# Kernel optimization log

Measured on AMD Instinct MI355X. Metric: run time of the kernel, lower is better.

## Reference

```python
import jax, jax.numpy as jnp
import numpy as np

H = 16          # num_attention_heads
HD = 64         # attention_head_size
ALPHA = 1.5
BANDWIDTH = 1.0
A_EXP = 0.5     # sinkhorn-like exponent 'a'
DIST_SCALE = float(HD)  # alpha < 2 => scale by head_size
EPS = 1e-12     # F.normalize eps


def setup_inputs() -> dict:
    key = jax.random.key(0)
    ks = jax.random.split(key, 5)
    B, L, D = 2, 1024, 1024
    w_scale = 0.02  # keep distances in a non-degenerate range for the power-law kernel
    x = jax.random.normal(ks[0], (B, L, D), dtype=jnp.float32)
    WQ = jax.random.normal(ks[1], (D, D), dtype=jnp.float32) * w_scale
    WK = jax.random.normal(ks[2], (D, D), dtype=jnp.float32) * w_scale
    WV = jax.random.normal(ks[3], (D, D), dtype=jnp.float32) * w_scale
    WO = jax.random.normal(ks[4], (D, D), dtype=jnp.float32) * w_scale
    z = jnp.zeros((D,), dtype=jnp.float32)
    return {"x": x, "WQ": WQ, "bQ": z, "WK": WK, "bK": z,
            "WV": WV, "bV": z, "WO": WO, "bO": z}


def _heads(t, B, L):
    # [B, L, H*HD] -> [B, H, L, HD]
    return t.reshape(B, L, H, HD).transpose(0, 2, 1, 3)


def reference(x, WQ, bQ, WK, bK, WV, bV, WO, bO):
    B, L, D = x.shape
    q = _heads(x @ WQ + bQ, B, L)   # [B,H,L,HD]
    k = _heads(x @ WK + bK, B, L)
    v = _heads(x @ WV + bV, B, L)

    # torch.cdist(q, k, p=2): pairwise euclidean distance [B,H,L,L]
    q2 = jnp.sum(q * q, axis=-1)                      # [B,H,L]
    k2 = jnp.sum(k * k, axis=-1)                      # [B,H,L]
    qk = jnp.einsum('bhid,bhjd->bhij', q, k)          # [B,H,L,L]
    d2 = q2[..., :, None] + k2[..., None, :] - 2.0 * qk
    g_dist = jnp.sqrt(jnp.maximum(d2, EPS)) / DIST_SCALE

    # alpha < 2: power-law kernel (1 + g/sqrt(bw))^(-(d_intrinsic + alpha))
    attn_score = (1.0 + g_dist / np.sqrt(BANDWIDTH)) ** (-(HD + ALPHA))

    # a > 0: Sinkhorn-style row/col renormalization
    N_R = jnp.sum(attn_score, axis=-1)                # [B,H,L] row sums
    N_C = jnp.sum(attn_score, axis=-2)                # [B,H,L] col sums
    K_tilde = (N_R ** (-A_EXP))[..., :, None] * attn_score * (N_C ** (-A_EXP))[..., None, :]

    # F.normalize(p=1, dim=3); entries are positive so |.| sum == sum
    attention_probs = K_tilde / jnp.maximum(jnp.sum(K_tilde, axis=-1, keepdims=True), EPS)

    out = jnp.einsum('bhij,bhjd->bhid', attention_probs, v)   # [B,H,L,HD]
    out = out.transpose(0, 2, 1, 3).reshape(B, L, H * HD)
    return out @ WO + bO
```

## Files before the change

### kernel.cpp

```cpp
#include <hip/hip_runtime.h>
#include <math.h>


typedef __attribute__((ext_vector_type(8))) short short8;
typedef __attribute__((ext_vector_type(4))) float f32x4;

__device__ inline unsigned short f2bf(float f) {
  unsigned int u = __float_as_uint(f);
  unsigned int r = (u + 0x7FFFu + ((u >> 16) & 1u)) >> 16;
  return (unsigned short)r;
}
__device__ inline float bf2f(unsigned short s) {
  return __uint_as_float(((unsigned int)s) << 16);
}
__device__ inline float score_fn(float dot, float sq) {
  float d2 = fmaxf(fmaf(-2.f, dot, sq), 1e-12f);
  float sd = __builtin_amdgcn_sqrtf(d2);
  float lg = __builtin_amdgcn_logf(fmaf(sd, 0.015625f, 1.0f));
  return __builtin_amdgcn_exp2f(-65.5f * lg);
}
__device__ inline unsigned int cvtpk(float lo, float hi) {
  unsigned int r;
  asm("v_cvt_pk_bf16_f32 %0, %1, %2" : "=v"(r) : "v"(lo), "v"(hi));
  return r;
}
#define GLD16(lptr, gptr)                                                      \
  __builtin_amdgcn_global_load_lds(                                            \
      (const __attribute__((address_space(1))) void*)(gptr),                   \
      (__attribute__((address_space(3))) void*)(lptr), 16, 0, 0)

__global__ __launch_bounds__(256) void cvt_f32_bf16(const float* __restrict__ in,
                                                    unsigned short* __restrict__ out) {
  int i = blockIdx.x * 256 + threadIdx.x;
  float4 v = ((const float4*)in)[i];
  out[4 * i + 0] = f2bf(v.x);
  out[4 * i + 1] = f2bf(v.y);
  out[4 * i + 2] = f2bf(v.z);
  out[4 * i + 3] = f2bf(v.w);
}

__global__ __launch_bounds__(256) void wtrans4(const float* __restrict__ W0,
                                               const float* __restrict__ W1,
                                               const float* __restrict__ W2,
                                               const float* __restrict__ W3,
                                               unsigned short* __restrict__ T0,
                                               unsigned short* __restrict__ T1,
                                               unsigned short* __restrict__ T2,
                                               unsigned short* __restrict__ T3) {
  int z = blockIdx.z;
  const float* W = z == 0 ? W0 : z == 1 ? W1 : z == 2 ? W2 : W3;
  unsigned short* WT = z == 0 ? T0 : z == 1 ? T1 : z == 2 ? T2 : T3;
  __shared__ float T[32][33];
  int k0 = blockIdx.x * 32, n0 = blockIdx.y * 32;
  int c = threadIdx.x & 31, r8 = threadIdx.x >> 5;
#pragma unroll
  for (int it = 0; it < 4; ++it) {
    int rr = r8 + it * 8;
    T[rr][c] = W[(size_t)(k0 + rr) * 1024 + n0 + c];
  }
  __syncthreads();
#pragma unroll
  for (int it = 0; it < 4; ++it) {
    int rr = r8 + it * 8;
    WT[(size_t)(n0 + rr) * 1024 + k0 + c] = f2bf(T[c][rr]);
  }
}

__global__ __launch_bounds__(512, 2) void gemm128k64(const unsigned short* __restrict__ A,
                                                     const unsigned short* __restrict__ B0,
                                                     const unsigned short* __restrict__ B1,
                                                     const unsigned short* __restrict__ B2,
                                                     const float* __restrict__ c0,
                                                     const float* __restrict__ c1,
                                                     const float* __restrict__ c2,
                                                     void* __restrict__ Y0,
                                                     void* __restrict__ Y1,
                                                     void* __restrict__ Y2,
                                                     int m0, int m1, int m2) {
  int z = blockIdx.z;
  const unsigned short* BT = z == 0 ? B0 : z == 1 ? B1 : B2;
  const float* bias = z == 0 ? c0 : z == 1 ? c1 : c2;
  void* Y = z == 0 ? Y0 : z == 1 ? Y1 : Y2;
  int mode = z == 0 ? m0 : z == 1 ? m1 : m2;

  __shared__ __align__(16) unsigned short As[2][128 * 64];
  __shared__ __align__(16) unsigned short Bs[2][128 * 64];
  int tid = threadIdx.x;
  int w = tid >> 6, l = tid & 63, g = l >> 4, l15 = l & 15;
  int wm = w >> 2, wn = w & 3;
  int bm = blockIdx.x * 128, bn = blockIdx.y * 128;
  const int x7 = l15 & 7;

  const int i0 = tid, i1 = tid + 512;
  const int r0 = i0 >> 3, s0 = (i0 & 7) ^ (r0 & 7);
  const int r1 = i1 >> 3, s1 = (i1 & 7) ^ (r1 & 7);

  GLD16(&As[0][i0 * 8], &A[(size_t)(bm + r0) * 1024 + s0 * 8]);
  GLD16(&As[0][i1 * 8], &A[(size_t)(bm + r1) * 1024 + s1 * 8]);
  GLD16(&Bs[0][i0 * 8], &BT[(size_t)(bn + r0) * 1024 + s0 * 8]);
  GLD16(&Bs[0][i1 * 8], &BT[(size_t)(bn + r1) * 1024 + s1 * 8]);

  f32x4 acc[4][2];
#pragma unroll
  for (int mi = 0; mi < 4; ++mi)
#pragma unroll
    for (int ni = 0; ni < 2; ++ni)
#pragma unroll
      for (int r = 0; r < 4; ++r) acc[mi][ni][r] = 0.f;

  __syncthreads();
  for (int t = 0; t < 16; ++t) {
    int cur = t & 1;
    if (t < 15) {
      int kn = (t + 1) * 64;
      GLD16(&As[cur ^ 1][i0 * 8], &A[(size_t)(bm + r0) * 1024 + kn + s0 * 8]);
      GLD16(&As[cur ^ 1][i1 * 8], &A[(size_t)(bm + r1) * 1024 + kn + s1 * 8]);
      GLD16(&Bs[cur ^ 1][i0 * 8], &BT[(size_t)(bn + r0) * 1024 + kn + s0 * 8]);
      GLD16(&Bs[cur ^ 1][i1 * 8], &BT[(size_t)(bn + r1) * 1024 + kn + s1 * 8]);
    }
#pragma unroll
    for (int kc = 0; kc < 2; ++kc) {
      const int cread = (((kc << 2) + g) ^ x7) * 8;
      short8 a[4], b[2];
#pragma unroll
      for (int mi = 0; mi < 4; ++mi)
        a[mi] = *(const short8*)&As[cur][(wm * 64 + mi * 16 + l15) * 64 + cread];
#pragma unroll
      for (int ni = 0; ni < 2; ++ni)
        b[ni] = *(const short8*)&Bs[cur][(wn * 32 + ni * 16 + l15) * 64 + cread];
#pragma unroll
      for (int mi = 0; mi < 4; ++mi)
#pragma unroll
        for (int ni = 0; ni < 2; ++ni)
          acc[mi][ni] = __builtin_amdgcn_mfma_f32_16x16x32_bf16(a[mi], b[ni], acc[mi][ni], 0, 0, 0);
    }
    __syncthreads();
  }

#pragma unroll
  for (int ni = 0; ni < 2; ++ni) {
    int n = bn + wn * 32 + ni * 16 + l15;
    float bv = bias[n];
#pragma unroll
    for (int mi = 0; mi < 4; ++mi) {
#pragma unroll
      for (int r = 0; r < 4; ++r) {
        int m = bm + wm * 64 + mi * 16 + 4 * g + r;
        float v = acc[mi][ni][r] + bv;
        if (mode == 0) {
          int b = m >> 10, ll = m & 1023, h = n >> 6, hd = n & 63;
          ((unsigned short*)Y)[(((size_t)(b * 16 + h) * 1024) + ll) * 64 + hd] = f2bf(v);
        } else if (mode == 1) {
          int b = m >> 10, ll = m & 1023, h = n >> 6, hd = n & 63;
          int jp = (ll & ~31) | (((ll >> 2) & 3) * 8 + ((ll >> 4) & 1) * 4 + (ll & 3));
          ((unsigned short*)Y)[(((size_t)(b * 16 + h) * 64) + hd) * 1024 + jp] = f2bf(v);
        } else {
          ((float*)Y)[(size_t)m * 1024 + n] = v;
        }
      }
    }
  }
}

__global__ __launch_bounds__(256) void gemm_st(const unsigned short* __restrict__ A,
                                               const unsigned short* __restrict__ B0,
                                               const unsigned short* __restrict__ B1,
                                               const unsigned short* __restrict__ B2,
                                               const float* __restrict__ c0,
                                               const float* __restrict__ c1,
                                               const float* __restrict__ c2,
                                               void* __restrict__ Y0,
                                               void* __restrict__ Y1,
                                               void* __restrict__ Y2,
                                               int m0, int m1, int m2) {
  int z = blockIdx.z;
  const unsigned short* BT = z == 0 ? B0 : z == 1 ? B1 : B2;
  const float* bias = z == 0 ? c0 : z == 1 ? c1 : c2;
  void* Y = z == 0 ? Y0 : z == 1 ? Y1 : Y2;
  int mode = z == 0 ? m0 : z == 1 ? m1 : m2;

  __shared__ __align__(16) unsigned short As[2][64 * 64];
  __shared__ __align__(16) unsigned short Bs[2][64 * 64];
  int tid = threadIdx.x;
  int w = tid >> 6, l = tid & 63, g = l >> 4, l15 = l & 15;
  int bm = blockIdx.x * 64, bn = blockIdx.y * 64;
  const int arow = w * 16 + l15;
  const int x7 = l15 & 7;

  const int i0s = tid, i1s = 256 + tid;
  const int r0 = i0s >> 3, s0 = (i0s & 7) ^ (r0 & 7);
  const int r1 = i1s >> 3, s1 = (i1s & 7) ^ (r1 & 7);

  GLD16(&As[0][i0s * 8], &A[(size_t)(bm + r0) * 1024 + s0 * 8]);
  GLD16(&As[0][i1s * 8], &A[(size_t)(bm + r1) * 1024 + s1 * 8]);
  GLD16(&Bs[0][i0s * 8], &BT[(size_t)(bn + r0) * 1024 + s0 * 8]);
  GLD16(&Bs[0][i1s * 8], &BT[(size_t)(bn + r1) * 1024 + s1 * 8]);

  f32x4 acc[4];
#pragma unroll
  for (int t = 0; t < 4; ++t)
#pragma unroll
    for (int r = 0; r < 4; ++r) acc[t][r] = 0.f;

  __syncthreads();
  for (int t = 0; t < 16; ++t) {
    int cur = t & 1;
    if (t < 15) {
      int kn = (t + 1) * 64;
      GLD16(&As[cur ^ 1][i0s * 8], &A[(size_t)(bm + r0) * 1024 + kn + s0 * 8]);
      GLD16(&As[cur ^ 1][i1s * 8], &A[(size_t)(bm + r1) * 1024 + kn + s1 * 8]);
      GLD16(&Bs[cur ^ 1][i0s * 8], &BT[(size_t)(bn + r0) * 1024 + kn + s0 * 8]);
      GLD16(&Bs[cur ^ 1][i1s * 8], &BT[(size_t)(bn + r1) * 1024 + kn + s1 * 8]);
    }
#pragma unroll
    for (int kc = 0; kc < 2; ++kc) {
      short8 a = *(const short8*)&As[cur][arow * 64 + ((kc * 4 + g) ^ x7) * 8];
#pragma unroll
      for (int tt = 0; tt < 4; ++tt) {
        short8 b = *(const short8*)&Bs[cur][(tt * 16 + l15) * 64 + ((kc * 4 + g) ^ x7) * 8];
        acc[tt] = __builtin_amdgcn_mfma_f32_16x16x32_bf16(a, b, acc[tt], 0, 0, 0);
      }
    }
    __syncthreads();
  }

#pragma unroll
  for (int t = 0; t < 4; ++t) {
    int n = bn + 16 * t + l15;
    float bv = bias[n];
#pragma unroll
    for (int r = 0; r < 4; ++r) {
      int m = bm + w * 16 + 4 * g + r;
      float v = acc[t][r] + bv;
      if (mode == 0) {
        int b = m >> 10, ll = m & 1023, h = n >> 6, hd = n & 63;
        ((unsigned short*)Y)[(((size_t)(b * 16 + h) * 1024) + ll) * 64 + hd] = f2bf(v);
      } else if (mode == 1) {
        int b = m >> 10, ll = m & 1023, h = n >> 6, hd = n & 63;
        int jp = (ll & ~31) | (((ll >> 2) & 3) * 8 + ((ll >> 4) & 1) * 4 + (ll & 3));
        ((unsigned short*)Y)[(((size_t)(b * 16 + h) * 64) + hd) * 1024 + jp] = f2bf(v);
      } else {
        ((float*)Y)[(size_t)m * 1024 + n] = v;
      }
    }
  }
}

__global__ __launch_bounds__(256) void sqnorm(const unsigned short* __restrict__ Qb,
                                              const unsigned short* __restrict__ Kb,
                                              float* __restrict__ q2,
                                              float* __restrict__ k2) {
  int row = blockIdx.x * 256 + threadIdx.x;
  const unsigned short* src = blockIdx.y ? Kb : Qb;
  float* dst = blockIdx.y ? k2 : q2;
  const short8* p = (const short8*)&src[(size_t)row * 64];
  float s = 0.f;
#pragma unroll
  for (int c = 0; c < 8; ++c) {
    short8 v = p[c];
#pragma unroll
    for (int e = 0; e < 8; ++e) {
      float f = bf2f((unsigned short)v[e]);
      s = fmaf(f, f, s);
    }
  }
  dst[row] = s;
}

__global__ __launch_bounds__(256) void colsum_mfma(const unsigned short* __restrict__ Qb,
                                                   const unsigned short* __restrict__ Kb,
                                                   const float* __restrict__ q2,
                                                   const float* __restrict__ k2,
                                                   float* __restrict__ rnc) {
  __shared__ __align__(16) unsigned short Qd[2][64 * 64];
  __shared__ __align__(16) float q2s[1024];
  int bh = blockIdx.x, jt = blockIdx.y;
  int tid = threadIdx.x, w = tid >> 6, l = tid & 63;
  int g = l >> 4, l15 = l & 15;
  const int x7 = l15 & 7;
  const unsigned short* Qp = Qb + (size_t)bh * 65536;
  const unsigned short* Kp = Kb + (size_t)bh * 65536;
  int j = jt * 64 + w * 16 + l15;

  const int i0s = tid, i1s = 256 + tid;
  const int r0 = i0s >> 3, s0 = (i0s & 7) ^ (r0 & 7);
  const int r1 = i1s >> 3, s1 = (i1s & 7) ^ (r1 & 7);

  GLD16(&q2s[tid * 4], q2 + (size_t)bh * 1024 + tid * 4);
  GLD16(&Qd[0][i0s * 8], Qp + (size_t)r0 * 64 + s0 * 8);
  GLD16(&Qd[0][i1s * 8], Qp + (size_t)r1 * 64 + s1 * 8);

  short8 bk0 = *(const short8*)&Kp[(size_t)j * 64 + 8 * g];
  short8 bk1 = *(const short8*)&Kp[(size_t)j * 64 + 32 + 8 * g];
  float k2j = k2[(size_t)bh * 1024 + j];
  float colacc = 0.f;

  __syncthreads();
  for (int t = 0; t < 16; ++t) {
    int cur = t & 1;
    if (t < 15) {
      int inx = (t + 1) * 64;
      GLD16(&Qd[cur ^ 1][i0s * 8], Qp + (size_t)(inx + r0) * 64 + s0 * 8);
      GLD16(&Qd[cur ^ 1][i1s * 8], Qp + (size_t)(inx + r1) * 64 + s1 * 8);
    }
    const unsigned short* Ql = Qd[cur];
#pragma unroll
    for (int tp = 0; tp < 4; ++tp) {
      int rowb = (16 * tp + l15) * 64;
      short8 a0 = *(const short8*)&Ql[rowb + ((g) ^ x7) * 8];
      short8 a1 = *(const short8*)&Ql[rowb + ((4 + g) ^ x7) * 8];
      f32x4 cf;
#pragma unroll
      for (int r = 0; r < 4; ++r) cf[r] = 0.f;
      cf = __builtin_amdgcn_mfma_f32_16x16x32_bf16(a0, bk0, cf, 0, 0, 0);
      cf = __builtin_amdgcn_mfma_f32_16x16x32_bf16(a1, bk1, cf, 0, 0, 0);
      float4 qv = *(const float4*)&q2s[t * 64 + 16 * tp + 4 * g];
      colacc += score_fn(cf[0], qv.x + k2j);
      colacc += score_fn(cf[1], qv.y + k2j);
      colacc += score_fn(cf[2], qv.z + k2j);
      colacc += score_fn(cf[3], qv.w + k2j);
    }
    __syncthreads();
  }
  colacc += __shfl_xor(colacc, 16);
  colacc += __shfl_xor(colacc, 32);
  if (l < 16) rnc[(size_t)bh * 1024 + jt * 64 + w * 16 + l] = __builtin_amdgcn_rsqf(colacc);
}

__global__ __launch_bounds__(256) void attn_mfma(const unsigned short* __restrict__ Qb,
                                                 const unsigned short* __restrict__ Kb,
                                                 const unsigned short* __restrict__ VTp,
                                                 const float* __restrict__ q2,
                                                 const float* __restrict__ k2,
                                                 const float* __restrict__ rnc,
                                                 unsigned short* __restrict__ AO) {
  __shared__ __align__(16) unsigned short Kd[2][64 * 64];
  __shared__ __align__(16) unsigned short Vd[2][64 * 64];
  __shared__ __align__(16) float k2s[1024];
  __shared__ __align__(16) float rns[1024];
  int bh = blockIdx.x;
  int tid = threadIdx.x, w = tid >> 6, l = tid & 63;
  int g = l >> 4, l15 = l & 15;
  const int x7 = l15 & 7;
  int it0 = blockIdx.y * 64 + w * 16;
  const unsigned short* Qp = Qb + (size_t)bh * 65536;
  const unsigned short* Kp = Kb + (size_t)bh * 65536;
  const unsigned short* Vp = VTp + (size_t)bh * 65536;
  int b = bh >> 4, h = bh & 15;

  const int i0s = tid, i1s = 256 + tid;
  const int r0 = i0s >> 3, s0 = (i0s & 7) ^ (r0 & 7);
  const int r1 = i1s >> 3, s1 = (i1s & 7) ^ (r1 & 7);

  GLD16(&k2s[tid * 4], k2 + (size_t)bh * 1024 + tid * 4);
  GLD16(&rns[tid * 4], rnc + (size_t)bh * 1024 + tid * 4);
  GLD16(&Kd[0][i0s * 8], Kp + (size_t)r0 * 64 + s0 * 8);
  GLD16(&Kd[0][i1s * 8], Kp + (size_t)r1 * 64 + s1 * 8);
  GLD16(&Vd[0][i0s * 8], Vp + (size_t)r0 * 1024 + s0 * 8);
  GLD16(&Vd[0][i1s * 8], Vp + (size_t)r1 * 1024 + s1 * 8);

  short8 bq0 = *(const short8*)&Qp[(size_t)(it0 + l15) * 64 + 8 * g];
  short8 bq1 = *(const short8*)&Qp[(size_t)(it0 + l15) * 64 + 32 + 8 * g];
  float q2l = q2[(size_t)bh * 1024 + it0 + l15];

  f32x4 o[4];
#pragma unroll
  for (int t = 0; t < 4; ++t)
#pragma unroll
    for (int r = 0; r < 4; ++r) o[t][r] = 0.f;
  float dacc = 0.f;

  __syncthreads();
  for (int t = 0; t < 16; ++t) {
    int cur = t & 1;
    if (t < 15) {
      int j0n = (t + 1) * 64;
      GLD16(&Kd[cur ^ 1][i0s * 8], Kp + (size_t)(j0n + r0) * 64 + s0 * 8);
      GLD16(&Kd[cur ^ 1][i1s * 8], Kp + (size_t)(j0n + r1) * 64 + s1 * 8);
      GLD16(&Vd[cur ^ 1][i0s * 8], Vp + (size_t)r0 * 1024 + j0n + s0 * 8);
      GLD16(&Vd[cur ^ 1][i1s * 8], Vp + (size_t)r1 * 1024 + j0n + s1 * 8);
    }
    const unsigned short* Kl = Kd[cur];
    const unsigned short* Vl = Vd[cur];
    int j0 = t * 64;
    float sc[16];
#pragma unroll
    for (int tp = 0; tp < 4; ++tp) {
      int rowb = (16 * tp + l15) * 64;
      short8 a0 = *(const short8*)&Kl[rowb + ((g) ^ x7) * 8];
      short8 a1 = *(const short8*)&Kl[rowb + ((4 + g) ^ x7) * 8];
      f32x4 cf;
#pragma unroll
      for (int r = 0; r < 4; ++r) cf[r] = 0.f;
      cf = __builtin_amdgcn_mfma_f32_16x16x32_bf16(a0, bq0, cf, 0, 0, 0);
      cf = __builtin_amdgcn_mfma_f32_16x16x32_bf16(a1, bq1, cf, 0, 0, 0);
      float4 kv = *(const float4*)&k2s[j0 + 16 * tp + 4 * g];
      float4 rv = *(const float4*)&rns[j0 + 16 * tp + 4 * g];
      sc[tp * 4 + 0] = score_fn(cf[0], q2l + kv.x) * rv.x;
      sc[tp * 4 + 1] = score_fn(cf[1], q2l + kv.y) * rv.y;
      sc[tp * 4 + 2] = score_fn(cf[2], q2l + kv.z) * rv.z;
      sc[tp * 4 + 3] = score_fn(cf[3], q2l + kv.w) * rv.w;
    }
#pragma unroll
    for (int i = 0; i < 16; ++i) dacc += sc[i];
    int pi0[4], pi1[4];
    pi0[0] = (int)cvtpk(sc[0], sc[1]);
    pi0[1] = (int)cvtpk(sc[2], sc[3]);
    pi0[2] = (int)cvtpk(sc[4], sc[5]);
    pi0[3] = (int)cvtpk(sc[6], sc[7]);
    pi1[0] = (int)cvtpk(sc[8], sc[9]);
    pi1[1] = (int)cvtpk(sc[10], sc[11]);
    pi1[2] = (int)cvtpk(sc[12], sc[13]);
    pi1[3] = (int)cvtpk(sc[14], sc[15]);
    short8 pa0 = *(short8*)pi0;
    short8 pa1 = *(short8*)pi1;
#pragma unroll
    for (int tt = 0; tt < 4; ++tt) {
      int rowb = (16 * tt + l15) * 64;
      short8 v0 = *(const short8*)&Vl[rowb + ((g) ^ x7) * 8];
      short8 v1 = *(const short8*)&Vl[rowb + ((4 + g) ^ x7) * 8];
      o[tt] = __builtin_amdgcn_mfma_f32_16x16x32_bf16(pa0, v0, o[tt], 0, 0, 0);
      o[tt] = __builtin_amdgcn_mfma_f32_16x16x32_bf16(pa1, v1, o[tt], 0, 0, 0);
    }
    __syncthreads();
  }

  dacc += __shfl_xor(dacc, 16);
  dacc += __shfl_xor(dacc, 32);
  float dv[4];
#pragma unroll
  for (int r = 0; r < 4; ++r) dv[r] = __shfl(dacc, 4 * g + r);

#pragma unroll
  for (int t = 0; t < 4; ++t) {
#pragma unroll
    for (int r = 0; r < 4; ++r) {
      int m = b * 1024 + it0 + 4 * g + r;
      int n = h * 64 + t * 16 + l15;
      AO[(size_t)m * 1024 + n] = f2bf(o[t][r] / dv[r]);
    }
  }
}

extern "C" void kernel_launch(void* const* d_in, const int* in_sizes, int n_in,
                              void* d_out, int out_size, void* d_ws, size_t ws_size,
                              hipStream_t stream) {
  const float* x  = (const float*)d_in[0];
  const float* WQ = (const float*)d_in[1];
  const float* bQ = (const float*)d_in[2];
  const float* WK = (const float*)d_in[3];
  const float* bK = (const float*)d_in[4];
  const float* WV = (const float*)d_in[5];
  const float* bV = (const float*)d_in[6];
  const float* WO = (const float*)d_in[7];
  const float* bO = (const float*)d_in[8];

  char* base = (char*)d_ws;
  unsigned short* xb  = (unsigned short*)(base);
  unsigned short* WQT = (unsigned short*)(base + (4u  << 20));
  unsigned short* WKT = (unsigned short*)(base + (6u  << 20));
  unsigned short* WVT = (unsigned short*)(base + (8u  << 20));
  unsigned short* WOT = (unsigned short*)(base + (10u << 20));
  unsigned short* Qb  = (unsigned short*)(base + (12u << 20));
  unsigned short* Kb  = (unsigned short*)(base + (16u << 20));
  unsigned short* VTp = (unsigned short*)(base + (20u << 20));
  unsigned short* AOb = (unsigned short*)(base + (24u << 20));
  float* q2  = (float*)(base + (28u << 20));
  float* k2  = (float*)(base + (28u << 20) + (128u << 10));
  float* rnc = (float*)(base + (28u << 20) + (256u << 10));

  cvt_f32_bf16<<<2048, 256, 0, stream>>>(x, xb);
  wtrans4<<<dim3(32, 32, 4), 256, 0, stream>>>(WQ, WK, WV, WO, WQT, WKT, WVT, WOT);

  gemm128k64<<<dim3(16, 8, 3), 512, 0, stream>>>(xb, WQT, WKT, WVT, bQ, bK, bV,
                                                 Qb, Kb, VTp, 0, 0, 1);

  sqnorm<<<dim3(128, 2), 256, 0, stream>>>(Qb, Kb, q2, k2);
  colsum_mfma<<<dim3(32, 16), 256, 0, stream>>>(Qb, Kb, q2, k2, rnc);
  attn_mfma<<<dim3(32, 16), 256, 0, stream>>>(Qb, Kb, VTp, q2, k2, rnc, AOb);

  gemm_st<<<dim3(32, 16, 1), 256, 0, stream>>>(AOb, WOT, WOT, WOT, bO, bO, bO,
                                               d_out, d_out, d_out, 2, 2, 2);
}
```

Before: 109.6 us.

## Fuse prep kernels, fold sqnorm into projection GEMM, widen attention K tiles

Merges the x conversion and weight transposes into a single prep launch. The projection GEMM epilogue now also computes per-head squared norms of the bf16 Q and K, which removes the separate sqnorm kernel. The colsum and attention kernels move from 64-key to 128-key LDS tiles with launch_bounds occupancy hints and s_setprio around the MFMAs, halving the number of loop iterations and barriers. gemm_st is specialised to plain fp32 output; the larger LDS footprint may lower occupancy.

```diff
diff --git a/kernel.cpp b/kernel.cpp
--- a/kernel.cpp
+++ b/kernel.cpp
@@ -29,29 +29,32 @@
       (const __attribute__((address_space(1))) void*)(gptr),                   \
       (__attribute__((address_space(3))) void*)(lptr), 16, 0, 0)
 
-__global__ __launch_bounds__(256) void cvt_f32_bf16(const float* __restrict__ in,
-                                                    unsigned short* __restrict__ out) {
-  int i = blockIdx.x * 256 + threadIdx.x;
-  float4 v = ((const float4*)in)[i];
-  out[4 * i + 0] = f2bf(v.x);
-  out[4 * i + 1] = f2bf(v.y);
-  out[4 * i + 2] = f2bf(v.z);
-  out[4 * i + 3] = f2bf(v.w);
-}
-
-__global__ __launch_bounds__(256) void wtrans4(const float* __restrict__ W0,
-                                               const float* __restrict__ W1,
-                                               const float* __restrict__ W2,
-                                               const float* __restrict__ W3,
-                                               unsigned short* __restrict__ T0,
-                                               unsigned short* __restrict__ T1,
-                                               unsigned short* __restrict__ T2,
-                                               unsigned short* __restrict__ T3) {
-  int z = blockIdx.z;
+__global__ __launch_bounds__(256) void prep(const float* __restrict__ x,
+                                            unsigned short* __restrict__ xb,
+                                            const float* __restrict__ W0,
+                                            const float* __restrict__ W1,
+                                            const float* __restrict__ W2,
+                                            const float* __restrict__ W3,
+                                            unsigned short* __restrict__ T0,
+                                            unsigned short* __restrict__ T1,
+                                            unsigned short* __restrict__ T2,
+                                            unsigned short* __restrict__ T3) {
+  __shared__ float T[32][33];
+  int bx = blockIdx.x;
+  if (bx < 2048) {
+    int i = bx * 256 + threadIdx.x;
+    float4 v = ((const float4*)x)[i];
+    xb[4 * i + 0] = f2bf(v.x);
+    xb[4 * i + 1] = f2bf(v.y);
+    xb[4 * i + 2] = f2bf(v.z);
+    xb[4 * i + 3] = f2bf(v.w);
+    return;
+  }
+  int idx = bx - 2048;
+  int z = idx >> 10, rem = idx & 1023;
   const float* W = z == 0 ? W0 : z == 1 ? W1 : z == 2 ? W2 : W3;
   unsigned short* WT = z == 0 ? T0 : z == 1 ? T1 : z == 2 ? T2 : T3;
-  __shared__ float T[32][33];
-  int k0 = blockIdx.x * 32, n0 = blockIdx.y * 32;
+  int k0 = (rem >> 5) * 32, n0 = (rem & 31) * 32;
   int c = threadIdx.x & 31, r8 = threadIdx.x >> 5;
 #pragma unroll
   for (int it = 0; it < 4; ++it) {
@@ -76,11 +79,15 @@
                                                      void* __restrict__ Y0,
                                                      void* __restrict__ Y1,
                                                      void* __restrict__ Y2,
+                                                     float* __restrict__ sq0,
+                                                     float* __restrict__ sq1,
+                                                     float* __restrict__ sq2,
                                                      int m0, int m1, int m2) {
   int z = blockIdx.z;
   const unsigned short* BT = z == 0 ? B0 : z == 1 ? B1 : B2;
   const float* bias = z == 0 ? c0 : z == 1 ? c1 : c2;
   void* Y = z == 0 ? Y0 : z == 1 ? Y1 : Y2;
+  float* sq = z == 0 ? sq0 : z == 1 ? sq1 : sq2;
   int mode = z == 0 ? m0 : z == 1 ? m1 : m2;
 
   __shared__ __align__(16) unsigned short As[2][128 * 64];
@@ -137,6 +144,12 @@
     __syncthreads();
   }
 
+  float rowsq[4][4];
+#pragma unroll
+  for (int mi = 0; mi < 4; ++mi)
+#pragma unroll
+    for (int r = 0; r < 4; ++r) rowsq[mi][r] = 0.f;
+
 #pragma unroll
   for (int ni = 0; ni < 2; ++ni) {
     int n = bn + wn * 32 + ni * 16 + l15;
@@ -149,7 +162,10 @@
         float v = acc[mi][ni][r] + bv;
         if (mode == 0) {
           int b = m >> 10, ll = m & 1023, h = n >> 6, hd = n & 63;
-          ((unsigned short*)Y)[(((size_t)(b * 16 + h) * 1024) + ll) * 64 + hd] = f2bf(v);
+          unsigned short ush = f2bf(v);
+          ((unsigned short*)Y)[(((size_t)(b * 16 + h) * 1024) + ll) * 64 + hd] = ush;
+          float f = bf2f(ush);
+          rowsq[mi][r] = fmaf(f, f, rowsq[mi][r]);
         } else if (mode == 1) {
           int b = m >> 10, ll = m & 1023, h = n >> 6, hd = n & 63;
           int jp = (ll & ~31) | (((ll >> 2) & 3) * 8 + ((ll >> 4) & 1) * 4 + (ll & 3));
@@ -160,25 +176,43 @@
       }
     }
   }
+
+  if (sq != nullptr) {
+    float* Sq = (float*)&As[0][0];
+#pragma unroll
+    for (int mi = 0; mi < 4; ++mi)
+#pragma unroll
+      for (int r = 0; r < 4; ++r) {
+        float s = rowsq[mi][r];
+        s += __shfl_xor(s, 1);
+        s += __shfl_xor(s, 2);
+        s += __shfl_xor(s, 4);
+        s += __shfl_xor(s, 8);
+        rowsq[mi][r] = s;
+      }
+    if (l15 == 0) {
+#pragma unroll
+      for (int mi = 0; mi < 4; ++mi)
+#pragma unroll
+        for (int r = 0; r < 4; ++r)
+          Sq[(wm * 4 + wn) * 64 + mi * 16 + 4 * g + r] = rowsq[mi][r];
+    }
+    __syncthreads();
+    if (tid < 256) {
+      int rr = tid & 127, hh = tid >> 7;
+      float s = Sq[((rr >> 6) * 4 + 2 * hh) * 64 + (rr & 63)] +
+                Sq[((rr >> 6) * 4 + 2 * hh + 1) * 64 + (rr & 63)];
+      int m = bm + rr, b = m >> 10, ll = m & 1023;
+      int h = (bn >> 6) + hh;
+      sq[(size_t)(b * 16 + h) * 1024 + ll] = s;
+    }
+  }
 }
 
 __global__ __launch_bounds__(256) void gemm_st(const unsigned short* __restrict__ A,
-                                               const unsigned short* __restrict__ B0,
-                                               const unsigned short* __restrict__ B1,
-                                               const unsigned short* __restrict__ B2,
-                                               const float* __restrict__ c0,
-                                               const float* __restrict__ c1,
-                                               const float* __restrict__ c2,
-                                               void* __restrict__ Y0,
-                                               void* __restrict__ Y1,
-                                               void* __restrict__ Y2,
-                                               int m0, int m1, int m2) {
-  int z = blockIdx.z;
-  const unsigned short* BT = z == 0 ? B0 : z == 1 ? B1 : B2;
-  const float* bias = z == 0 ? c0 : z == 1 ? c1 : c2;
-  void* Y = z == 0 ? Y0 : z == 1 ? Y1 : Y2;
-  int mode = z == 0 ? m0 : z == 1 ? m1 : m2;
-
+                                               const unsigned short* __restrict__ BT,
+                                               const float* __restrict__ bias,
+                                               float* __restrict__ Y) {
   __shared__ __align__(16) unsigned short As[2][64 * 64];
   __shared__ __align__(16) unsigned short Bs[2][64 * 64];
   int tid = threadIdx.x;
@@ -231,48 +265,17 @@
 #pragma unroll
     for (int r = 0; r < 4; ++r) {
       int m = bm + w * 16 + 4 * g + r;
-      float v = acc[t][r] + bv;
-      if (mode == 0) {
-        int b = m >> 10, ll = m & 1023, h = n >> 6, hd = n & 63;
-        ((unsigned short*)Y)[(((size_t)(b * 16 + h) * 1024) + ll) * 64 + hd] = f2bf(v);
-      } else if (mode == 1) {
-        int b = m >> 10, ll = m & 1023, h = n >> 6, hd = n & 63;
-        int jp = (ll & ~31) | (((ll >> 2) & 3) * 8 + ((ll >> 4) & 1) * 4 + (ll & 3));
-        ((unsigned short*)Y)[(((size_t)(b * 16 + h) * 64) + hd) * 1024 + jp] = f2bf(v);
-      } else {
-        ((float*)Y)[(size_t)m * 1024 + n] = v;
-      }
-    }
-  }
-}
-
-__global__ __launch_bounds__(256) void sqnorm(const unsigned short* __restrict__ Qb,
-                                              const unsigned short* __restrict__ Kb,
-                                              float* __restrict__ q2,
-                                              float* __restrict__ k2) {
-  int row = blockIdx.x * 256 + threadIdx.x;
-  const unsigned short* src = blockIdx.y ? Kb : Qb;
-  float* dst = blockIdx.y ? k2 : q2;
-  const short8* p = (const short8*)&src[(size_t)row * 64];
-  float s = 0.f;
-#pragma unroll
-  for (int c = 0; c < 8; ++c) {
-    short8 v = p[c];
-#pragma unroll
-    for (int e = 0; e < 8; ++e) {
-      float f = bf2f((unsigned short)v[e]);
-      s = fmaf(f, f, s);
-    }
-  }
-  dst[row] = s;
-}
-
-__global__ __launch_bounds__(256) void colsum_mfma(const unsigned short* __restrict__ Qb,
-                                                   const unsigned short* __restrict__ Kb,
-                                                   const float* __restrict__ q2,
-                                                   const float* __restrict__ k2,
-                                                   float* __restrict__ rnc) {
-  __shared__ __align__(16) unsigned short Qd[2][64 * 64];
+      Y[(size_t)m * 1024 + n] = acc[t][r] + bv;
+    }
+  }
+}
+
+__global__ __launch_bounds__(256, 2) void colsum_mfma(const unsigned short* __restrict__ Qb,
+                                                      const unsigned short* __restrict__ Kb,
+                                                      const float* __restrict__ q2,
+                                                      const float* __restrict__ k2,
+                                                      float* __restrict__ rnc) {
+  __shared__ __align__(16) unsigned short Qd[2][128 * 64];
   __shared__ __align__(16) float q2s[1024];
   int bh = blockIdx.x, jt = blockIdx.y;
   int tid = threadIdx.x, w = tid >> 6, l = tid & 63;
@@ -282,13 +285,18 @@
   const unsigned short* Kp = Kb + (size_t)bh * 65536;
   int j = jt * 64 + w * 16 + l15;
 
-  const int i0s = tid, i1s = 256 + tid;
-  const int r0 = i0s >> 3, s0 = (i0s & 7) ^ (r0 & 7);
-  const int r1 = i1s >> 3, s1 = (i1s & 7) ^ (r1 & 7);
+  int rQ[4], sQ[4];
+#pragma unroll
+  for (int it = 0; it < 4; ++it) {
+    int c = tid + 256 * it;
+    rQ[it] = c >> 3;
+    sQ[it] = (c & 7) ^ (rQ[it] & 7);
+  }
 
   GLD16(&q2s[tid * 4], q2 + (size_t)bh * 1024 + tid * 4);
-  GLD16(&Qd[0][i0s * 8], Qp + (size_t)r0 * 64 + s0 * 8);
-  GLD16(&Qd[0][i1s * 8], Qp + (size_t)r1 * 64 + s1 * 8);
+#pragma unroll
+  for (int it = 0; it < 4; ++it)
+    GLD16(&Qd[0][(tid + 256 * it) * 8], Qp + (size_t)rQ[it] * 64 + sQ[it] * 8);
 
   short8 bk0 = *(const short8*)&Kp[(size_t)j * 64 + 8 * g];
   short8 bk1 = *(const short8*)&Kp[(size_t)j * 64 + 32 + 8 * g];
@@ -296,25 +304,28 @@
   float colacc = 0.f;
 
   __syncthreads();
-  for (int t = 0; t < 16; ++t) {
+  for (int t = 0; t < 8; ++t) {
     int cur = t & 1;
-    if (t < 15) {
-      int inx = (t + 1) * 64;
-      GLD16(&Qd[cur ^ 1][i0s * 8], Qp + (size_t)(inx + r0) * 64 + s0 * 8);
-      GLD16(&Qd[cur ^ 1][i1s * 8], Qp + (size_t)(inx + r1) * 64 + s1 * 8);
+    if (t < 7) {
+      int inx = (t + 1) * 128;
+#pragma unroll
+      for (int it = 0; it < 4; ++it)
+        GLD16(&Qd[cur ^ 1][(tid + 256 * it) * 8], Qp + (size_t)(inx + rQ[it]) * 64 + sQ[it] * 8);
     }
     const unsigned short* Ql = Qd[cur];
 #pragma unroll
-    for (int tp = 0; tp < 4; ++tp) {
+    for (int tp = 0; tp < 8; ++tp) {
       int rowb = (16 * tp + l15) * 64;
       short8 a0 = *(const short8*)&Ql[rowb + ((g) ^ x7) * 8];
       short8 a1 = *(const short8*)&Ql[rowb + ((4 + g) ^ x7) * 8];
       f32x4 cf;
 #pragma unroll
       for (int r = 0; r < 4; ++r) cf[r] = 0.f;
+      __builtin_amdgcn_s_setprio(1);
       cf = __builtin_amdgcn_mfma_f32_16x16x32_bf16(a0, bk0, cf, 0, 0, 0);
       cf = __builtin_amdgcn_mfma_f32_16x16x32_bf16(a1, bk1, cf, 0, 0, 0);
-      float4 qv = *(const float4*)&q2s[t * 64 + 16 * tp + 4 * g];
+      __builtin_amdgcn_s_setprio(0);
+      float4 qv = *(const float4*)&q2s[t * 128 + 16 * tp + 4 * g];
       colacc += score_fn(cf[0], qv.x + k2j);
       colacc += score_fn(cf[1], qv.y + k2j);
       colacc += score_fn(cf[2], qv.z + k2j);
@@ -327,15 +338,15 @@
   if (l < 16) rnc[(size_t)bh * 1024 + jt * 64 + w * 16 + l] = __builtin_amdgcn_rsqf(colacc);
 }
 
-__global__ __launch_bounds__(256) void attn_mfma(const unsigned short* __restrict__ Qb,
-                                                 const unsigned short* __restrict__ Kb,
-                                                 const unsigned short* __restrict__ VTp,
-                                                 const float* __restrict__ q2,
-                                                 const float* __restrict__ k2,
-                                                 const float* __restrict__ rnc,
-                                                 unsigned short* __restrict__ AO) {
-  __shared__ __align__(16) unsigned short Kd[2][64 * 64];
-  __shared__ __align__(16) unsigned short Vd[2][64 * 64];
+__global__ __launch_bounds__(256, 2) void attn_mfma(const unsigned short* __restrict__ Qb,
+                                                    const unsigned short* __restrict__ Kb,
+                                                    const unsigned short* __restrict__ VTp,
+                                                    const float* __restrict__ q2,
+                                                    const float* __restrict__ k2,
+                                                    const float* __restrict__ rnc,
+                                                    unsigned short* __restrict__ AO) {
+  __shared__ __align__(16) unsigned short Kd[2][128 * 64];
+  __shared__ __align__(16) unsigned short Vd[2][64 * 128];
   __shared__ __align__(16) float k2s[1024];
   __shared__ __align__(16) float rns[1024];
   int bh = blockIdx.x;
@@ -348,16 +359,24 @@
   const unsigned short* Vp = VTp + (size_t)bh * 65536;
   int b = bh >> 4, h = bh & 15;
 
-  const int i0s = tid, i1s = 256 + tid;
-  const int r0 = i0s >> 3, s0 = (i0s & 7) ^ (r0 & 7);
-  const int r1 = i1s >> 3, s1 = (i1s & 7) ^ (r1 & 7);
+  int rK[4], cK[4], rV[4], cV[4];
+#pragma unroll
+  for (int it = 0; it < 4; ++it) {
+    int c = tid + 256 * it;
+    rK[it] = c >> 3;
+    cK[it] = ((c & 7) ^ (rK[it] & 7));
+    rV[it] = c >> 4;
+    int s = c & 15;
+    cV[it] = (s & 8) | ((s & 7) ^ (rV[it] & 7));
+  }
 
   GLD16(&k2s[tid * 4], k2 + (size_t)bh * 1024 + tid * 4);
   GLD16(&rns[tid * 4], rnc + (size_t)bh * 1024 + tid * 4);
-  GLD16(&Kd[0][i0s * 8], Kp + (size_t)r0 * 64 + s0 * 8);
-  GLD16(&Kd[0][i1s * 8], Kp + (size_t)r1 * 64 + s1 * 8);
-  GLD16(&Vd[0][i0s * 8], Vp + (size_t)r0 * 1024 + s0 * 8);
-  GLD16(&Vd[0][i1s * 8], Vp + (size_t)r1 * 1024 + s1 * 8);
+#pragma unroll
+  for (int it = 0; it < 4; ++it) {
+    GLD16(&Kd[0][(tid + 256 * it) * 8], Kp + (size_t)rK[it] * 64 + cK[it] * 8);
+    GLD16(&Vd[0][(tid + 256 * it) * 8], Vp + (size_t)rV[it] * 1024 + cV[it] * 8);
+  }
 
   short8 bq0 = *(const short8*)&Qp[(size_t)(it0 + l15) * 64 + 8 * g];
   short8 bq1 = *(const short8*)&Qp[(size_t)(it0 + l15) * 64 + 32 + 8 * g];
@@ -371,56 +390,64 @@
   float dacc = 0.f;
 
   __syncthreads();
-  for (int t = 0; t < 16; ++t) {
+  for (int t = 0; t < 8; ++t) {
     int cur = t & 1;
-    if (t < 15) {
-      int j0n = (t + 1) * 64;
-      GLD16(&Kd[cur ^ 1][i0s * 8], Kp + (size_t)(j0n + r0) * 64 + s0 * 8);
-      GLD16(&Kd[cur ^ 1][i1s * 8], Kp + (size_t)(j0n + r1) * 64 + s1 * 8);
-      GLD16(&Vd[cur ^ 1][i0s * 8], Vp + (size_t)r0 * 1024 + j0n + s0 * 8);
-      GLD16(&Vd[cur ^ 1][i1s * 8], Vp + (size_t)r1 * 1024 + j0n + s1 * 8);
+    if (t < 7) {
+      int j0n = (t + 1) * 128;
+#pragma unroll
+      for (int it = 0; it < 4; ++it) {
+        GLD16(&Kd[cur ^ 1][(tid + 256 * it) * 8], Kp + (size_t)(j0n + rK[it]) * 64 + cK[it] * 8);
+        GLD16(&Vd[cur ^ 1][(tid + 256 * it) * 8], Vp + (size_t)rV[it] * 1024 + j0n + cV[it] * 8);
+      }
     }
     const unsigned short* Kl = Kd[cur];
     const unsigned short* Vl = Vd[cur];
-    int j0 = t * 64;
-    float sc[16];
-#pragma unroll
-    for (int tp = 0; tp < 4; ++tp) {
-      int rowb = (16 * tp + l15) * 64;
-      short8 a0 = *(const short8*)&Kl[rowb + ((g) ^ x7) * 8];
-      short8 a1 = *(const short8*)&Kl[rowb + ((4 + g) ^ x7) * 8];
-      f32x4 cf;
-#pragma unroll
-      for (int r = 0; r < 4; ++r) cf[r] = 0.f;
-      cf = __builtin_amdgcn_mfma_f32_16x16x32_bf16(a0, bq0, cf, 0, 0, 0);
-      cf = __builtin_amdgcn_mfma_f32_16x16x32_bf16(a1, bq1, cf, 0, 0, 0);
-      float4 kv = *(const float4*)&k2s[j0 + 16 * tp + 4 * g];
-      float4 rv = *(const float4*)&rns[j0 + 16 * tp + 4 * g];
-      sc[tp * 4 + 0] = score_fn(cf[0], q2l + kv.x) * rv.x;
-      sc[tp * 4 + 1] = score_fn(cf[1], q2l + kv.y) * rv.y;
-      sc[tp * 4 + 2] = score_fn(cf[2], q2l + kv.z) * rv.z;
-      sc[tp * 4 + 3] = score_fn(cf[3], q2l + kv.w) * rv.w;
-    }
-#pragma unroll
-    for (int i = 0; i < 16; ++i) dacc += sc[i];
-    int pi0[4], pi1[4];
-    pi0[0] = (int)cvtpk(sc[0], sc[1]);
-    pi0[1] = (int)cvtpk(sc[2], sc[3]);
-    pi0[2] = (int)cvtpk(sc[4], sc[5]);
-    pi0[3] = (int)cvtpk(sc[6], sc[7]);
-    pi1[0] = (int)cvtpk(sc[8], sc[9]);
-    pi1[1] = (int)cvtpk(sc[10], sc[11]);
-    pi1[2] = (int)cvtpk(sc[12], sc[13]);
-    pi1[3] = (int)cvtpk(sc[14], sc[15]);
-    short8 pa0 = *(short8*)pi0;
-    short8 pa1 = *(short8*)pi1;
-#pragma unroll
-    for (int tt = 0; tt < 4; ++tt) {
-      int rowb = (16 * tt + l15) * 64;
-      short8 v0 = *(const short8*)&Vl[rowb + ((g) ^ x7) * 8];
-      short8 v1 = *(const short8*)&Vl[rowb + ((4 + g) ^ x7) * 8];
-      o[tt] = __builtin_amdgcn_mfma_f32_16x16x32_bf16(pa0, v0, o[tt], 0, 0, 0);
-      o[tt] = __builtin_amdgcn_mfma_f32_16x16x32_bf16(pa1, v1, o[tt], 0, 0, 0);
+#pragma unroll
+    for (int jj = 0; jj < 2; ++jj) {
+      float sc[16];
+#pragma unroll
+      for (int tp = 0; tp < 4; ++tp) {
+        int rowb = (jj * 64 + 16 * tp + l15) * 64;
+        short8 a0 = *(const short8*)&Kl[rowb + ((g) ^ x7) * 8];
+        short8 a1 = *(const short8*)&Kl[rowb + ((4 + g) ^ x7) * 8];
+        f32x4 cf;
+#pragma unroll
+        for (int r = 0; r < 4; ++r) cf[r] = 0.f;
+        __builtin_amdgcn_s_setprio(1);
+        cf = __builtin_amdgcn_mfma_f32_16x16x32_bf16(a0, bq0, cf, 0, 0, 0);
+        cf = __builtin_amdgcn_mfma_f32_16x16x32_bf16(a1, bq1, cf, 0, 0, 0);
+        __builtin_amdgcn_s_setprio(0);
+        int base = t * 128 + jj * 64 + 16 * tp + 4 * g;
+        float4 kv = *(const float4*)&k2s[base];
+        float4 rv = *(const float4*)&rns[base];
+        sc[tp * 4 + 0] = score_fn(cf[0], q2l + kv.x) * rv.x;
+        sc[tp * 4 + 1] = score_fn(cf[1], q2l + kv.y) * rv.y;
+        sc[tp * 4 + 2] = score_fn(cf[2], q2l + kv.z) * rv.z;
+        sc[tp * 4 + 3] = score_fn(cf[3], q2l + kv.w) * rv.w;
+      }
+#pragma unroll
+      for (int i = 0; i < 16; ++i) dacc += sc[i];
+      int pi0[4], pi1[4];
+      pi0[0] = (int)cvtpk(sc[0], sc[1]);
+      pi0[1] = (int)cvtpk(sc[2], sc[3]);
+      pi0[2] = (int)cvtpk(sc[4], sc[5]);
+      pi0[3] = (int)cvtpk(sc[6], sc[7]);
+      pi1[0] = (int)cvtpk(sc[8], sc[9]);
+      pi1[1] = (int)cvtpk(sc[10], sc[11]);
+      pi1[2] = (int)cvtpk(sc[12], sc[13]);
+      pi1[3] = (int)cvtpk(sc[14], sc[15]);
+      short8 pa0 = *(short8*)pi0;
+      short8 pa1 = *(short8*)pi1;
+#pragma unroll
+      for (int t5 = 0; t5 < 4; ++t5) {
+        int vr = 16 * t5 + l15;
+        short8 bv0 = *(const short8*)&Vl[vr * 128 + (jj * 8 + ((g) ^ x7)) * 8];
+        short8 bv1 = *(const short8*)&Vl[vr * 128 + (jj * 8 + ((4 + g) ^ x7)) * 8];
+        __builtin_amdgcn_s_setprio(1);
+        o[t5] = __builtin_amdgcn_mfma_f32_16x16x32_bf16(pa0, bv0, o[t5], 0, 0, 0);
+        o[t5] = __builtin_amdgcn_mfma_f32_16x16x32_bf16(pa1, bv1, o[t5], 0, 0, 0);
+        __builtin_amdgcn_s_setprio(0);
+      }
     }
     __syncthreads();
   }
@@ -469,16 +496,14 @@
   float* k2  = (float*)(base + (28u << 20) + (128u << 10));
   float* rnc = (float*)(base + (28u << 20) + (256u << 10));
 
-  cvt_f32_bf16<<<2048, 256, 0, stream>>>(x, xb);
-  wtrans4<<<dim3(32, 32, 4), 256, 0, stream>>>(WQ, WK, WV, WO, WQT, WKT, WVT, WOT);
+  prep<<<6144, 256, 0, stream>>>(x, xb, WQ, WK, WV, WO, WQT, WKT, WVT, WOT);
 
   gemm128k64<<<dim3(16, 8, 3), 512, 0, stream>>>(xb, WQT, WKT, WVT, bQ, bK, bV,
-                                                 Qb, Kb, VTp, 0, 0, 1);
-
-  sqnorm<<<dim3(128, 2), 256, 0, stream>>>(Qb, Kb, q2, k2);
+                                                 Qb, Kb, VTp, q2, k2, nullptr,
+                                                 0, 0, 1);
+
   colsum_mfma<<<dim3(32, 16), 256, 0, stream>>>(Qb, Kb, q2, k2, rnc);
   attn_mfma<<<dim3(32, 16), 256, 0, stream>>>(Qb, Kb, VTp, q2, k2, rnc, AOb);
 
-  gemm_st<<<dim3(32, 16, 1), 256, 0, stream>>>(AOb, WOT, WOT, WOT, bO, bO, bO,
-                                               d_out, d_out, d_out, 2, 2, 2);
-}
+  gemm_st<<<dim3(32, 16), 256, 0, stream>>>(AOb, WOT, bO, (float*)d_out);
+}
```

After: 98.72 us. 1.11x faster.
